# Performance work log

Measured on AMD Instinct MI355X. Metric: run time of the kernel, lower is better.

The kernel has to match this reference:

```python
import jax, jax.numpy as jnp
import numpy as np

VOCAB = 30522
EMB = 128
H = 128          # per-direction GRU hidden (text_hidden_size // 2)
TXT = 256        # text_hidden_size
VDIM = 1024      # visual_feature_dim
VHID = 256       # video_hidden_dim
ADIM = 256       # alignment_dim
REG = 0.05
N_ITERS = 10


def gru_seq(x, Wi, Wh, bi, bh):
    """PyTorch-convention GRU. x:(B,T,I), Wi:(3H,I), Wh:(3H,H). Returns (B,T,H)."""
    B, T, _ = x.shape
    Hd = Wh.shape[1]
    xg = jnp.einsum('bti,gi->btg', x, Wi) + bi  # precompute input gates (B,T,3H)

    def step(h, xg_t):
        hg = h @ Wh.T + bh
        xr, xz, xn = jnp.split(xg_t, 3, axis=-1)
        hr, hz, hn = jnp.split(hg, 3, axis=-1)
        r = jax.nn.sigmoid(xr + hr)
        z = jax.nn.sigmoid(xz + hz)
        n = jnp.tanh(xn + r * hn)
        h_new = (1.0 - z) * n + z * h
        return h_new, h_new

    h0 = jnp.zeros((B, Hd), x.dtype)
    _, hs = jax.lax.scan(step, h0, jnp.swapaxes(xg, 0, 1))
    return jnp.swapaxes(hs, 0, 1)


def mlp_scorer(x, W1, b1, w2, b2, act):
    h = act(jnp.einsum('bsd,hd->bsh', x, W1) + b1)
    return jax.nn.sigmoid(jnp.einsum('bsh,h->bs', h, w2) + b2)


def sinkhorn(E, V, reg=REG, num_iters=N_ITERS):
    B, K, _ = E.shape
    M = V.shape[1]
    En = E / (jnp.linalg.norm(E, axis=-1, keepdims=True) + 1e-12)
    Vn = V / (jnp.linalg.norm(V, axis=-1, keepdims=True) + 1e-12)
    C = 1.0 - jnp.einsum('bkd,bmd->bkm', En, Vn)
    Km = jnp.exp(-C / reg)
    mu = jnp.full((B, K), 1.0 / K, E.dtype)
    nu = jnp.full((B, M), 1.0 / M, E.dtype)
    u = jnp.full((B, K), 1.0 / K, E.dtype)
    v = jnp.full((B, M), 1.0 / M, E.dtype)
    for _ in range(num_iters):
        u = mu / (jnp.einsum('bkm,bm->bk', Km, v) + 1e-8)
        v = nu / (jnp.einsum('bkm,bk->bm', Km, u) + 1e-8)
    T = u[:, :, None] * Km * v[:, None, :]
    dist = jnp.sum(T * C) / B
    return dist, T


def setup_inputs() -> dict:
    key = jax.random.key(0)
    ks = jax.random.split(key, 24)
    B, S, W, M = 16, 128, 32, 256
    s = 0.02
    inp = {
        'input_ids': jax.random.randint(ks[0], (B, S, W), 0, VOCAB),
        'attention_mask': jnp.ones((B, S, W), jnp.int64 if jax.config.jax_enable_x64 else jnp.int32),
        'video_features': jax.random.normal(ks[1], (B, M, VDIM), jnp.float32),
        'emb': jax.random.normal(ks[2], (VOCAB, EMB), jnp.float32) * s,
        'gru_Wi_f': jax.random.normal(ks[3], (3 * H, EMB), jnp.float32) * s,
        'gru_Wh_f': jax.random.normal(ks[4], (3 * H, H), jnp.float32) * s,
        'gru_bi_f': jnp.zeros((3 * H,), jnp.float32),
        'gru_bh_f': jnp.zeros((3 * H,), jnp.float32),
        'gru_Wi_b': jax.random.normal(ks[5], (3 * H, EMB), jnp.float32) * s,
        'gru_Wh_b': jax.random.normal(ks[6], (3 * H, H), jnp.float32) * s,
        'gru_bi_b': jnp.zeros((3 * H,), jnp.float32),
        'gru_bh_b': jnp.zeros((3 * H,), jnp.float32),
        'tproj_W': jax.random.normal(ks[7], (ADIM, TXT), jnp.float32) * s,
        'tproj_b': jnp.zeros((ADIM,), jnp.float32),
        'vproj_W': jax.random.normal(ks[8], (ADIM, VDIM), jnp.float32) * s,
        'vproj_b': jnp.zeros((ADIM,), jnp.float32),
        'tsum_W1': jax.random.normal(ks[9], (H, TXT), jnp.float32) * s,
        'tsum_b1': jnp.zeros((H,), jnp.float32),
        'tsum_w2': jax.random.normal(ks[10], (H,), jnp.float32) * s,
        'tsum_b2': jnp.zeros((), jnp.float32),
        'vsum_W1': jax.random.normal(ks[11], (VHID, VDIM), jnp.float32) * s,
        'vsum_b1': jnp.zeros((VHID,), jnp.float32),
        'vsum_w2': jax.random.normal(ks[12], (VHID,), jnp.float32) * s,
        'vsum_b2': jnp.zeros((), jnp.float32),
        'vts_W1': jax.random.normal(ks[13], (VHID, VDIM), jnp.float32) * s,
        'vts_b1': jnp.zeros((VHID,), jnp.float32),
        'vts_w2': jax.random.normal(ks[14], (VHID,), jnp.float32) * s,
        'vts_b2': jnp.zeros((), jnp.float32),
    }
    return inp


def reference(input_ids, attention_mask, video_features, emb,
              gru_Wi_f, gru_Wh_f, gru_bi_f, gru_bh_f,
              gru_Wi_b, gru_Wh_b, gru_bi_b, gru_bh_b,
              tproj_W, tproj_b, vproj_W, vproj_b,
              tsum_W1, tsum_b1, tsum_w2, tsum_b2,
              vsum_W1, vsum_b1, vsum_w2, vsum_b2,
              vts_W1, vts_b1, vts_w2, vts_b2):
    B, S, W = input_ids.shape
    flat = input_ids.reshape(B * S, W)
    embeds = emb[flat]  # (B*S, W, EMB); padding_idx=0 row is just a table row here
    fwd = gru_seq(embeds, gru_Wi_f, gru_Wh_f, gru_bi_f, gru_bh_f)
    bwd = gru_seq(embeds[:, ::-1, :], gru_Wi_b, gru_Wh_b, gru_bi_b, gru_bh_b)[:, ::-1, :]
    gru_out = jnp.concatenate([fwd, bwd], axis=-1)  # (B*S, W, 2H)
    text_features = gru_out.mean(axis=1).reshape(B, S, TXT)

    text_seg_probs = jnp.zeros((B, S), text_features.dtype)
    video_seg_probs = mlp_scorer(video_features, vts_W1, vts_b1, vts_w2, vts_b2, jax.nn.relu)
    text_summ_probs = mlp_scorer(text_features, tsum_W1, tsum_b1, tsum_w2, tsum_b2, jnp.tanh)
    video_summ_probs = mlp_scorer(video_features, vsum_W1, vsum_b1, vsum_w2, vsum_b2, jnp.tanh)

    E_w = text_features * text_summ_probs[:, :, None]
    V_w = video_features * video_summ_probs[:, :, None]
    E_proj = jnp.einsum('bsd,ad->bsa', E_w, tproj_W) + tproj_b
    V_proj = jnp.einsum('bmd,ad->bma', V_w, vproj_W) + vproj_b

    ot_loss, T = sinkhorn(E_proj, V_proj)
    return (text_seg_probs, text_features, video_seg_probs, text_summ_probs,
            video_summ_probs, ot_loss, T)
```

## Files before the change

### kernel.cpp

```cpp
#include <hip/hip_runtime.h>
#include <hip/hip_bf16.h>

typedef unsigned short u16;
typedef __attribute__((ext_vector_type(8))) short short8;
typedef __attribute__((ext_vector_type(4))) float f32x4;

static __device__ __forceinline__ float bf2f(u16 x) {
    unsigned int u = ((unsigned int)x) << 16;
    return __uint_as_float(u);
}
static __device__ __forceinline__ u16 f2bf(float f) {
    unsigned int u = __float_as_uint(f);
    unsigned int r = (u + 0x7fffu + ((u >> 16) & 1u)) >> 16;
    return (u16)r;
}
static __device__ __forceinline__ float sigmoidf(float x) {
    return 1.0f / (1.0f + expf(-x));
}

__global__ void k_zero(float* __restrict__ out) {
    int t = blockIdx.x * 256 + threadIdx.x;
    if (t < 2048) out[t] = 0.0f;
    if (t == 0) out[536576] = 0.0f;
}

__global__ void k_cvte(const float* __restrict__ emb, const float* __restrict__ WiF,
                       const float* __restrict__ WiB, u16* __restrict__ dst) {
    long i4 = ((long)blockIdx.x * 256 + threadIdx.x) * 4;
    if (i4 >= 4005120) return;
    float4 v;
    if (i4 < 3906816) v = *(const float4*)(emb + i4);
    else if (i4 < 3955968) v = *(const float4*)(WiF + (i4 - 3906816));
    else v = *(const float4*)(WiB + (i4 - 3955968));
    ushort4 o;
    o.x = f2bf(v.x); o.y = f2bf(v.y); o.z = f2bf(v.z); o.w = f2bf(v.w);
    *(ushort4*)(dst + i4) = o;
}

__global__ __launch_bounds__(256) void k_xg2(const int* __restrict__ ids, const u16* __restrict__ embb,
                                             const u16* __restrict__ Wib, const float* __restrict__ bi,
                                             u16* __restrict__ xg) {
    __shared__ u16 As[128][40];
    __shared__ u16 Bs[128][40];
    const int t = threadIdx.x;
    const int m0 = blockIdx.x * 128, n0 = blockIdx.y * 128;
    const int w = t >> 6, l = t & 63;
    const int wr = w >> 1, wc = w & 1;
    const int lrow = l & 15, lk = (l >> 4) * 8;
    f32x4 acc[4][4] = {};
#pragma unroll
    for (int kk = 0; kk < 4; kk++) {
        const int k0 = kk * 32;
        int4 ra[2], rb[2];
#pragma unroll
        for (int it = 0; it < 2; it++) {
            int e = it * 256 + t;
            int row = e >> 2, c8 = (e & 3) * 8;
            int id = ids[m0 + row];
            ra[it] = *(const int4*)(embb + (long)id * 128 + k0 + c8);
            rb[it] = *(const int4*)(Wib + (long)(n0 + row) * 128 + k0 + c8);
        }
        __syncthreads();
#pragma unroll
        for (int it = 0; it < 2; it++) {
            int e = it * 256 + t;
            int row = e >> 2, c8 = (e & 3) * 8;
            *(int4*)&As[row][c8] = ra[it];
            *(int4*)&Bs[row][c8] = rb[it];
        }
        __syncthreads();
        short8 af[4], bf[4];
#pragma unroll
        for (int f = 0; f < 4; f++) {
            af[f] = *(const short8*)&As[wr * 64 + f * 16 + lrow][lk];
            bf[f] = *(const short8*)&Bs[wc * 64 + f * 16 + lrow][lk];
        }
#pragma unroll
        for (int fm = 0; fm < 4; fm++)
#pragma unroll
            for (int fn = 0; fn < 4; fn++)
                acc[fm][fn] = __builtin_amdgcn_mfma_f32_16x16x32_bf16(af[fm], bf[fn], acc[fm][fn], 0, 0, 0);
    }
    const int orow = (l >> 4) * 4, ocol = l & 15;
#pragma unroll
    for (int fm = 0; fm < 4; fm++)
#pragma unroll
        for (int fn = 0; fn < 4; fn++) {
            const int col = n0 + wc * 64 + fn * 16 + ocol;
            const float bbv = bi[col];
            const int row0 = m0 + wr * 64 + fm * 16 + orow;
#pragma unroll
            for (int r = 0; r < 4; r++)
                xg[(long)(row0 + r) * 384 + col] = f2bf(acc[fm][fn][r] + bbv);
        }
}

__global__ __launch_bounds__(256) void k_scan2(const u16* __restrict__ xg,
                                               const float* __restrict__ Wh,
                                               const float* __restrict__ bh,
                                               float* __restrict__ tf_out, int dir) {
    __shared__ u16 hbuf[2][16][136];
    const int t = threadIdx.x;
    const int w = t >> 6, l = t & 63;
    const int lr = l & 15, hi = l >> 4;
    const int seq0 = blockIdx.x * 8;

    short8 breg[3][2][4];
    float bb[3][2];
#pragma unroll
    for (int g = 0; g < 3; g++)
#pragma unroll
        for (int h2 = 0; h2 < 2; h2++) {
            const int ncol = g * 128 + w * 32 + h2 * 16 + lr;
            const float* wrow = Wh + (long)ncol * 128;
            bb[g][h2] = bh[ncol];
#pragma unroll
            for (int q = 0; q < 4; q++) {
                float4 a = *(const float4*)(wrow + q * 32 + hi * 8);
                float4 b = *(const float4*)(wrow + q * 32 + hi * 8 + 4);
                short8 s;
                s[0] = f2bf(a.x); s[1] = f2bf(a.y); s[2] = f2bf(a.z); s[3] = f2bf(a.w);
                s[4] = f2bf(b.x); s[5] = f2bf(b.y); s[6] = f2bf(b.z); s[7] = f2bf(b.w);
                breg[g][h2][q] = s;
            }
        }

    for (int i = t; i < 2176; i += 256) ((int*)hbuf)[i] = 0;

    float hreg[2][4] = {};
    float macc[2][4] = {};
    __syncthreads();

    for (int tt = 0; tt < 32; tt++) {
        const int tp = dir ? (31 - tt) : tt;
        const int cur = tt & 1;

        float xv[3][2][4];
        if (hi < 2) {
#pragma unroll
            for (int g = 0; g < 3; g++)
#pragma unroll
                for (int h2 = 0; h2 < 2; h2++)
#pragma unroll
                    for (int r = 0; r < 4; r++) {
                        const int m = hi * 4 + r;
                        xv[g][h2][r] = bf2f(xg[((long)(seq0 + m) * 32 + tp) * 384
                                               + g * 128 + w * 32 + h2 * 16 + lr]);
                    }
        }

        short8 af[4];
#pragma unroll
        for (int q = 0; q < 4; q++)
            af[q] = *(const short8*)&hbuf[cur][lr][q * 32 + hi * 8];

        f32x4 acc[3][2];
#pragma unroll
        for (int g = 0; g < 3; g++)
#pragma unroll
            for (int h2 = 0; h2 < 2; h2++) {
                f32x4 a = {0.f, 0.f, 0.f, 0.f};
#pragma unroll
                for (int q = 0; q < 4; q++)
                    a = __builtin_amdgcn_mfma_f32_16x16x32_bf16(af[q], breg[g][h2][q], a, 0, 0, 0);
                acc[g][h2] = a;
            }

        if (hi < 2) {
#pragma unroll
            for (int h2 = 0; h2 < 2; h2++)
#pragma unroll
                for (int r = 0; r < 4; r++) {
                    float rg = sigmoidf(xv[0][h2][r] + acc[0][h2][r] + bb[0][h2]);
                    float zg = sigmoidf(xv[1][h2][r] + acc[1][h2][r] + bb[1][h2]);
                    float ng = tanhf(xv[2][h2][r] + rg * (acc[2][h2][r] + bb[2][h2]));
                    float h = (1.0f - zg) * ng + zg * hreg[h2][r];
                    hreg[h2][r] = h;
                    macc[h2][r] += h;
                    hbuf[cur ^ 1][hi * 4 + r][w * 32 + h2 * 16 + lr] = f2bf(h);
                }
        }
        __syncthreads();
    }

    if (hi < 2) {
#pragma unroll
        for (int h2 = 0; h2 < 2; h2++)
#pragma unroll
            for (int r = 0; r < 4; r++)
                tf_out[(long)(seq0 + hi * 4 + r) * 256 + dir * 128 + w * 32 + h2 * 16 + lr]
                    = macc[h2][r] * (1.0f / 32.0f);
    }
}

__global__ void k_tsum(const float* __restrict__ tf, const float* __restrict__ W1,
                       const float* __restrict__ b1, const float* __restrict__ w2,
                       const float* __restrict__ b2, float* __restrict__ out) {
    __shared__ float x[256];
    __shared__ float wsum[2];
    const int row = blockIdx.x, t = threadIdx.x;
    x[t] = tf[(long)row * 256 + t];
    x[t + 128] = tf[(long)row * 256 + 128 + t];
    __syncthreads();
    float acc = 0.f;
    const float* w = W1 + (long)t * 256;
#pragma unroll 8
    for (int i = 0; i < 256; i += 4) {
        float4 w4 = *(const float4*)(w + i);
        acc += w4.x * x[i] + w4.y * x[i + 1] + w4.z * x[i + 2] + w4.w * x[i + 3];
    }
    float h = tanhf(acc + b1[t]) * w2[t];
    for (int o = 32; o > 0; o >>= 1) h += __shfl_xor(h, o);
    if ((t & 63) == 0) wsum[t >> 6] = h;
    __syncthreads();
    if (t == 0) out[row] = sigmoidf(wsum[0] + wsum[1] + b2[0]);
}

__global__ void k_cvt(const float* __restrict__ vf, const float* __restrict__ wa,
                      const float* __restrict__ wb2, const float* __restrict__ wc2,
                      u16* __restrict__ Xb, u16* __restrict__ Wb) {
    long gid = (long)blockIdx.x * 256 + threadIdx.x;
    long i4 = gid * 4;
    float4 v;
    u16* dst;
    if (i4 < 4194304) {
        v = *(const float4*)(vf + i4);
        dst = Xb + i4;
    } else {
        long j = i4 - 4194304;
        dst = Wb + j;
        if (j < 262144) v = *(const float4*)(wa + j);
        else if (j < 524288) v = *(const float4*)(wb2 + (j - 262144));
        else v = *(const float4*)(wc2 + (j - 524288));
    }
    ushort4 o;
    o.x = f2bf(v.x); o.y = f2bf(v.y); o.z = f2bf(v.z); o.w = f2bf(v.w);
    *(ushort4*)dst = o;
}

__global__ __launch_bounds__(256) void k_gemmv(const u16* __restrict__ Xb, const u16* __restrict__ Wb,
                                               float* __restrict__ G) {
    __shared__ u16 As[128][40];
    __shared__ u16 Bs[128][40];
    const int t = threadIdx.x;
    const int m0 = blockIdx.x * 128, n0 = blockIdx.y * 128;
    const int w = t >> 6, l = t & 63;
    const int wr = w >> 1, wc = w & 1;
    const int lrow = l & 15, lk = (l >> 4) * 8;
    f32x4 acc[4][4] = {};
    for (int kk = 0; kk < 32; kk++) {
        const int k0 = kk * 32;
        int4 ra[2], rb[2];
#pragma unroll
        for (int it = 0; it < 2; it++) {
            int e = it * 256 + t;
            int row = e >> 2, c8 = (e & 3) * 8;
            ra[it] = *(const int4*)(Xb + (long)(m0 + row) * 1024 + k0 + c8);
            rb[it] = *(const int4*)(Wb + (long)(n0 + row) * 1024 + k0 + c8);
        }
        __syncthreads();
#pragma unroll
        for (int it = 0; it < 2; it++) {
            int e = it * 256 + t;
            int row = e >> 2, c8 = (e & 3) * 8;
            *(int4*)&As[row][c8] = ra[it];
            *(int4*)&Bs[row][c8] = rb[it];
        }
        __syncthreads();
        short8 af[4], bf[4];
#pragma unroll
        for (int f = 0; f < 4; f++) {
            af[f] = *(const short8*)&As[wr * 64 + f * 16 + lrow][lk];
            bf[f] = *(const short8*)&Bs[wc * 64 + f * 16 + lrow][lk];
        }
#pragma unroll
        for (int fm = 0; fm < 4; fm++)
#pragma unroll
            for (int fn = 0; fn < 4; fn++)
                acc[fm][fn] = __builtin_amdgcn_mfma_f32_16x16x32_bf16(af[fm], bf[fn], acc[fm][fn], 0, 0, 0);
    }
    const int orow = (l >> 4) * 4, ocol = l & 15;
#pragma unroll
    for (int fm = 0; fm < 4; fm++)
#pragma unroll
        for (int fn = 0; fn < 4; fn++) {
            long base = (long)(m0 + wr * 64 + fm * 16 + orow) * 768 + n0 + wc * 64 + fn * 16 + ocol;
#pragma unroll
            for (int r = 0; r < 4; r++)
                G[base + (long)r * 768] = acc[fm][fn][r];
        }
}

__global__ void k_vepi(const float* __restrict__ G,
                       const float* __restrict__ bv, const float* __restrict__ w2v, const float* __restrict__ b2v,
                       const float* __restrict__ bt, const float* __restrict__ w2t, const float* __restrict__ b2t,
                       const float* __restrict__ vpb,
                       float* __restrict__ V, float* __restrict__ vsp, float* __restrict__ vseg) {
    const int r = blockIdx.x * 4 + (threadIdx.x >> 6);
    const int lane = threadIdx.x & 63;
    const float* g = G + (long)r * 768;
    float s1 = 0.f, s2 = 0.f;
#pragma unroll
    for (int c = 0; c < 4; c++) {
        int h = lane + c * 64;
        s1 += tanhf(g[h] + bv[h]) * w2v[h];
        s2 += fmaxf(g[256 + h] + bt[h], 0.0f) * w2t[h];
    }
    for (int o = 32; o > 0; o >>= 1) { s1 += __shfl_xor(s1, o); s2 += __shfl_xor(s2, o); }
    float p = sigmoidf(s1 + b2v[0]);
    if (lane == 0) {
        vsp[r] = p;
        vseg[r] = sigmoidf(s2 + b2t[0]);
    }
#pragma unroll
    for (int c = 0; c < 4; c++) {
        int a = lane + c * 64;
        V[(long)r * 256 + a] = vpb[a] + p * g[512 + a];
    }
}

__global__ void k_eproj(const float* __restrict__ tf, const float* __restrict__ tsp,
                        const float* __restrict__ W, const float* __restrict__ b,
                        float* __restrict__ E) {
    __shared__ float x[8][256];
    __shared__ float p[8];
    const int r0 = blockIdx.x * 8, t = threadIdx.x;
    const float4* src = (const float4*)(tf + (long)r0 * 256);
    for (int i = t; i < 512; i += 256) ((float4*)&x[0][0])[i] = src[i];
    if (t < 8) p[t] = tsp[r0 + t];
    __syncthreads();
    float acc[8] = {};
    const float* w = W + (long)t * 256;
    for (int i = 0; i < 256; i += 4) {
        float4 w4 = *(const float4*)(w + i);
#pragma unroll
        for (int r = 0; r < 8; r++) {
            float4 x4 = *(const float4*)&x[r][i];
            acc[r] += w4.x * x4.x + w4.y * x4.y + w4.z * x4.z + w4.w * x4.w;
        }
    }
    const float bb = b[t];
#pragma unroll
    for (int r = 0; r < 8; r++) E[(long)(r0 + r) * 256 + t] = bb + p[r] * acc[r];
}

__global__ void k_norm(float* __restrict__ E, float* __restrict__ V) {
    const int w = threadIdx.x >> 6, lane = threadIdx.x & 63;
    const int row = blockIdx.x * 4 + w;
    float* ptr = (row < 2048) ? (E + (long)row * 256) : (V + (long)(row - 2048) * 256);
    float4 v = ((float4*)ptr)[lane];
    float s = v.x * v.x + v.y * v.y + v.z * v.z + v.w * v.w;
    for (int o = 32; o > 0; o >>= 1) s += __shfl_xor(s, o);
    float sc = 1.0f / (sqrtf(s) + 1e-12f);
    v.x *= sc; v.y *= sc; v.z *= sc; v.w *= sc;
    ((float4*)ptr)[lane] = v;
}

__global__ void k_cost(const float* __restrict__ E, const float* __restrict__ V,
                       float* __restrict__ C, float* __restrict__ Km) {
    __shared__ float en[16][256];
    const int b = blockIdx.x, k0 = blockIdx.y * 16, t = threadIdx.x;
    const float4* esrc = (const float4*)(E + ((long)b * 128 + k0) * 256);
    for (int i = t; i < 1024; i += 256) ((float4*)&en[0][0])[i] = esrc[i];
    __syncthreads();
    float acc[16] = {};
    const float* vrow = V + ((long)b * 256 + t) * 256;
    for (int i = 0; i < 256; i += 4) {
        float4 v4 = *(const float4*)(vrow + i);
#pragma unroll
        for (int k = 0; k < 16; k++) {
            float4 e4 = *(const float4*)&en[k][i];
            acc[k] += e4.x * v4.x + e4.y * v4.y + e4.z * v4.z + e4.w * v4.w;
        }
    }
#pragma unroll
    for (int k = 0; k < 16; k++) {
        float c = 1.0f - acc[k];
        long idx = (long)b * 32768 + (long)(k0 + k) * 256 + t;
        C[idx] = c;
        Km[idx] = expf(-20.0f * c);
    }
}

__global__ void k_sink(const float* __restrict__ C, const float* __restrict__ Km,
                       float* __restrict__ T, float* __restrict__ loss) {
    __shared__ float u[128];
    __shared__ float v[256];
    __shared__ float red[8];
    const int b = blockIdx.x, t = threadIdx.x;
    const float* Kb = Km + (long)b * 32768;
    const float* Cb = C + (long)b * 32768;
    if (t < 128) u[t] = 1.0f / 128.0f;
    if (t < 256) v[t] = 1.0f / 256.0f;
    __syncthreads();
    for (int it = 0; it < 10; it++) {
        {
            const int k = t >> 2, q = t & 3;
            const float* kr = Kb + (long)k * 256 + q * 64;
            float s = 0.f;
#pragma unroll 4
            for (int m = 0; m < 64; m += 4) {
                float4 k4 = *(const float4*)(kr + m);
                float4 vv = *(const float4*)&v[q * 64 + m];
                s += k4.x * vv.x + k4.y * vv.y + k4.z * vv.z + k4.w * vv.w;
            }
            s += __shfl_xor(s, 1);
            s += __shfl_xor(s, 2);
            float un = (1.0f / 128.0f) / (s + 1e-8f);
            u[k] = un;
            __syncthreads();
        }
        {
            const int m = t >> 1, q = t & 1;
            float s = 0.f;
            for (int k = 0; k < 64; k += 4) {
                float4 u4 = *(const float4*)&u[q * 64 + k];
                s += Kb[(long)(q * 64 + k + 0) * 256 + m] * u4.x;
                s += Kb[(long)(q * 64 + k + 1) * 256 + m] * u4.y;
                s += Kb[(long)(q * 64 + k + 2) * 256 + m] * u4.z;
                s += Kb[(long)(q * 64 + k + 3) * 256 + m] * u4.w;
            }
            s += __shfl_xor(s, 1);
            float vn = (1.0f / 256.0f) / (s + 1e-8f);
            v[m] = vn;
            __syncthreads();
        }
    }
    float part = 0.f;
    for (int i = 0; i < 64; i++) {
        int idx = i * 512 + t;
        int k = idx >> 8, m = idx & 255;
        float tv = u[k] * Kb[idx] * v[m];
        T[(long)b * 32768 + idx] = tv;
        part += tv * Cb[idx];
    }
    for (int o = 32; o > 0; o >>= 1) part += __shfl_xor(part, o);
    if ((t & 63) == 0) red[t >> 6] = part;
    __syncthreads();
    if (t == 0) {
        float s = red[0] + red[1] + red[2] + red[3] + red[4] + red[5] + red[6] + red[7];
        atomicAdd(loss, s * (1.0f / 16.0f));
    }
}

extern "C" void kernel_launch(void* const* d_in, const int* in_sizes, int n_in,
                              void* d_out, int out_size, void* d_ws, size_t ws_size,
                              hipStream_t stream) {
    const int*   ids  = (const int*)d_in[0];
    const float* vf   = (const float*)d_in[2];
    const float* emb  = (const float*)d_in[3];
    const float* WiF  = (const float*)d_in[4];
    const float* WhF  = (const float*)d_in[5];
    const float* biF  = (const float*)d_in[6];
    const float* bhF  = (const float*)d_in[7];
    const float* WiB  = (const float*)d_in[8];
    const float* WhB  = (const float*)d_in[9];
    const float* biB  = (const float*)d_in[10];
    const float* bhB  = (const float*)d_in[11];
    const float* tpW  = (const float*)d_in[12];
    const float* tpb  = (const float*)d_in[13];
    const float* vpW  = (const float*)d_in[14];
    const float* vpb  = (const float*)d_in[15];
    const float* tsW1 = (const float*)d_in[16];
    const float* tsb1 = (const float*)d_in[17];
    const float* tsw2 = (const float*)d_in[18];
    const float* tsb2 = (const float*)d_in[19];
    const float* vsW1 = (const float*)d_in[20];
    const float* vsb1 = (const float*)d_in[21];
    const float* vsw2 = (const float*)d_in[22];
    const float* vsb2 = (const float*)d_in[23];
    const float* vtW1 = (const float*)d_in[24];
    const float* vtb1 = (const float*)d_in[25];
    const float* vtw2 = (const float*)d_in[26];
    const float* vtb2 = (const float*)d_in[27];
    float* out = (float*)d_out;

    char* ws = (char*)d_ws;
    u16*   XG = (u16*)ws;
    u16*   Xb = (u16*)ws;
    u16*   Wb = (u16*)(ws + 8388608);
    float* G  = (float*)(ws + 9961472);
    u16*   embb = (u16*)(ws + 50331648);
    u16*   WibF = embb + 3906816;
    u16*   WibB = embb + 3955968;
    float* E  = (float*)(ws + 50331648);
    float* V  = (float*)(ws + 52428800);
    float* C  = (float*)(ws + 56623104);
    float* Km = (float*)(ws + 58720256);

    float* tf   = out + 2048;
    float* vseg = out + 526336;
    float* tsp  = out + 530432;
    float* vsp  = out + 532480;
    float* loss = out + 536576;
    float* T    = out + 536577;

    k_zero<<<8, 256, 0, stream>>>(out);

    k_cvte<<<3912, 256, 0, stream>>>(emb, WiF, WiB, embb);
    k_xg2<<<dim3(512, 3), 256, 0, stream>>>(ids, embb, WibF, biF, XG);
    k_scan2<<<256, 256, 0, stream>>>(XG, WhF, bhF, tf, 0);
    k_xg2<<<dim3(512, 3), 256, 0, stream>>>(ids, embb, WibB, biB, XG);
    k_scan2<<<256, 256, 0, stream>>>(XG, WhB, bhB, tf, 1);

    k_cvt<<<4864, 256, 0, stream>>>(vf, vsW1, vtW1, vpW, Xb, Wb);
    k_gemmv<<<dim3(32, 6), 256, 0, stream>>>(Xb, Wb, G);
    k_vepi<<<1024, 256, 0, stream>>>(G, vsb1, vsw2, vsb2, vtb1, vtw2, vtb2, vpb, V, vsp, vseg);

    k_tsum<<<2048, 128, 0, stream>>>(tf, tsW1, tsb1, tsw2, tsb2, tsp);
    k_eproj<<<256, 256, 0, stream>>>(tf, tsp, tpW, tpb, E);
    k_norm<<<1536, 256, 0, stream>>>(E, V);
    k_cost<<<dim3(16, 8), 256, 0, stream>>>(E, V, C, Km);
    k_sink<<<16, 512, 0, stream>>>(C, Km, T, loss);
}
```

Before: 572.7 us.

## Restructure GRU scan with time-major xg, LDS prefetch, 8 waves, fast math

The input-gate projection is now written time-major, so each scan step reads one contiguous slab of 8 sequences. The scan block is doubled to 512 threads (8 waves), each owning 16 hidden columns. The next timestep's gates are prefetched into a double-buffered LDS tile while the current step computes, which takes scattered global loads off the serial recurrence. Sigmoid, tanh and exp switch to fast-intrinsic versions throughout, trading some accuracy for shorter latency.

```diff
diff --git a/kernel.cpp b/kernel.cpp
--- a/kernel.cpp
+++ b/kernel.cpp
@@ -16,6 +16,12 @@
 }
 static __device__ __forceinline__ float sigmoidf(float x) {
     return 1.0f / (1.0f + expf(-x));
+}
+static __device__ __forceinline__ float fsig(float x) {
+    return __fdividef(1.0f, 1.0f + __expf(-x));
+}
+static __device__ __forceinline__ float ftanh(float x) {
+    return 1.0f - __fdividef(2.0f, 1.0f + __expf(2.0f * x));
 }
 
 __global__ void k_zero(float* __restrict__ out) {
@@ -39,7 +45,7 @@
 
 __global__ __launch_bounds__(256) void k_xg2(const int* __restrict__ ids, const u16* __restrict__ embb,
                                              const u16* __restrict__ Wib, const float* __restrict__ bi,
-                                             u16* __restrict__ xg) {
+                                             u16* __restrict__ xgt) {
     __shared__ u16 As[128][40];
     __shared__ u16 Bs[128][40];
     const int t = threadIdx.x;
@@ -90,106 +96,100 @@
             const float bbv = bi[col];
             const int row0 = m0 + wr * 64 + fm * 16 + orow;
 #pragma unroll
-            for (int r = 0; r < 4; r++)
-                xg[(long)(row0 + r) * 384 + col] = f2bf(acc[fm][fn][r] + bbv);
-        }
-}
-
-__global__ __launch_bounds__(256) void k_scan2(const u16* __restrict__ xg,
+            for (int r = 0; r < 4; r++) {
+                const int mrow = row0 + r;
+                xgt[((long)(mrow & 31) * 2048 + (mrow >> 5)) * 384 + col]
+                    = f2bf(acc[fm][fn][r] + bbv);
+            }
+        }
+}
+
+__global__ __launch_bounds__(512) void k_scan3(const u16* __restrict__ xgt,
                                                const float* __restrict__ Wh,
                                                const float* __restrict__ bh,
                                                float* __restrict__ tf_out, int dir) {
-    __shared__ u16 hbuf[2][16][136];
+    __shared__ u16 hbuf[2][16][140];
+    __shared__ u16 xbuf[2][8][392];
     const int t = threadIdx.x;
     const int w = t >> 6, l = t & 63;
     const int lr = l & 15, hi = l >> 4;
     const int seq0 = blockIdx.x * 8;
 
-    short8 breg[3][2][4];
-    float bb[3][2];
-#pragma unroll
-    for (int g = 0; g < 3; g++)
-#pragma unroll
-        for (int h2 = 0; h2 < 2; h2++) {
-            const int ncol = g * 128 + w * 32 + h2 * 16 + lr;
-            const float* wrow = Wh + (long)ncol * 128;
-            bb[g][h2] = bh[ncol];
-#pragma unroll
-            for (int q = 0; q < 4; q++) {
-                float4 a = *(const float4*)(wrow + q * 32 + hi * 8);
-                float4 b = *(const float4*)(wrow + q * 32 + hi * 8 + 4);
-                short8 s;
-                s[0] = f2bf(a.x); s[1] = f2bf(a.y); s[2] = f2bf(a.z); s[3] = f2bf(a.w);
-                s[4] = f2bf(b.x); s[5] = f2bf(b.y); s[6] = f2bf(b.z); s[7] = f2bf(b.w);
-                breg[g][h2][q] = s;
-            }
-        }
-
-    for (int i = t; i < 2176; i += 256) ((int*)hbuf)[i] = 0;
-
-    float hreg[2][4] = {};
-    float macc[2][4] = {};
+    short8 breg[3][4];
+    float bb[3];
+#pragma unroll
+    for (int g = 0; g < 3; g++) {
+        const int ncol = g * 128 + w * 16 + lr;
+        const float* wrow = Wh + (long)ncol * 128;
+        bb[g] = bh[ncol];
+#pragma unroll
+        for (int q = 0; q < 4; q++) {
+            float4 a = *(const float4*)(wrow + q * 32 + hi * 8);
+            float4 b = *(const float4*)(wrow + q * 32 + hi * 8 + 4);
+            short8 s;
+            s[0] = f2bf(a.x); s[1] = f2bf(a.y); s[2] = f2bf(a.z); s[3] = f2bf(a.w);
+            s[4] = f2bf(b.x); s[5] = f2bf(b.y); s[6] = f2bf(b.z); s[7] = f2bf(b.w);
+            breg[g][q] = s;
+        }
+    }
+    for (int i = t; i < 2240; i += 512) ((int*)hbuf)[i] = 0;
+    const int seqr = t / 48, part = t % 48;
+    if (t < 384) {
+        const int tp0 = dir ? 31 : 0;
+        *(int4*)&xbuf[0][seqr][part * 8] =
+            *(const int4*)(xgt + ((long)tp0 * 2048 + seq0 + seqr) * 384 + part * 8);
+    }
+    float hreg[4] = {0.f, 0.f, 0.f, 0.f};
+    float macc[4] = {0.f, 0.f, 0.f, 0.f};
     __syncthreads();
 
     for (int tt = 0; tt < 32; tt++) {
-        const int tp = dir ? (31 - tt) : tt;
         const int cur = tt & 1;
-
-        float xv[3][2][4];
-        if (hi < 2) {
-#pragma unroll
-            for (int g = 0; g < 3; g++)
-#pragma unroll
-                for (int h2 = 0; h2 < 2; h2++)
-#pragma unroll
-                    for (int r = 0; r < 4; r++) {
-                        const int m = hi * 4 + r;
-                        xv[g][h2][r] = bf2f(xg[((long)(seq0 + m) * 32 + tp) * 384
-                                               + g * 128 + w * 32 + h2 * 16 + lr]);
-                    }
-        }
-
+        int4 pre;
+        const bool do_pre = (tt < 31) && (t < 384);
+        if (do_pre) {
+            const int tpn = dir ? (30 - tt) : (tt + 1);
+            pre = *(const int4*)(xgt + ((long)tpn * 2048 + seq0 + seqr) * 384 + part * 8);
+        }
         short8 af[4];
 #pragma unroll
         for (int q = 0; q < 4; q++)
             af[q] = *(const short8*)&hbuf[cur][lr][q * 32 + hi * 8];
-
-        f32x4 acc[3][2];
-#pragma unroll
-        for (int g = 0; g < 3; g++)
-#pragma unroll
-            for (int h2 = 0; h2 < 2; h2++) {
-                f32x4 a = {0.f, 0.f, 0.f, 0.f};
-#pragma unroll
-                for (int q = 0; q < 4; q++)
-                    a = __builtin_amdgcn_mfma_f32_16x16x32_bf16(af[q], breg[g][h2][q], a, 0, 0, 0);
-                acc[g][h2] = a;
+        f32x4 acc[3];
+#pragma unroll
+        for (int g = 0; g < 3; g++) {
+            f32x4 a = {0.f, 0.f, 0.f, 0.f};
+#pragma unroll
+            for (int q = 0; q < 4; q++)
+                a = __builtin_amdgcn_mfma_f32_16x16x32_bf16(af[q], breg[g][q], a, 0, 0, 0);
+            acc[g] = a;
+        }
+        if (hi < 2) {
+            const int c = w * 16 + lr;
+#pragma unroll
+            for (int r = 0; r < 4; r++) {
+                const int m = hi * 4 + r;
+                float xr = bf2f(xbuf[cur][m][c]);
+                float xz = bf2f(xbuf[cur][m][128 + c]);
+                float xn = bf2f(xbuf[cur][m][256 + c]);
+                float rg = fsig(xr + acc[0][r] + bb[0]);
+                float zg = fsig(xz + acc[1][r] + bb[1]);
+                float ng = ftanh(xn + rg * (acc[2][r] + bb[2]));
+                float h = (1.0f - zg) * ng + zg * hreg[r];
+                hreg[r] = h;
+                macc[r] += h;
+                hbuf[cur ^ 1][m][c] = f2bf(h);
             }
-
-        if (hi < 2) {
-#pragma unroll
-            for (int h2 = 0; h2 < 2; h2++)
-#pragma unroll
-                for (int r = 0; r < 4; r++) {
-                    float rg = sigmoidf(xv[0][h2][r] + acc[0][h2][r] + bb[0][h2]);
-                    float zg = sigmoidf(xv[1][h2][r] + acc[1][h2][r] + bb[1][h2]);
-                    float ng = tanhf(xv[2][h2][r] + rg * (acc[2][h2][r] + bb[2][h2]));
-                    float h = (1.0f - zg) * ng + zg * hreg[h2][r];
-                    hreg[h2][r] = h;
-                    macc[h2][r] += h;
-                    hbuf[cur ^ 1][hi * 4 + r][w * 32 + h2 * 16 + lr] = f2bf(h);
-                }
-        }
+        }
+        if (do_pre) *(int4*)&xbuf[cur ^ 1][seqr][part * 8] = pre;
         __syncthreads();
     }
 
     if (hi < 2) {
 #pragma unroll
-        for (int h2 = 0; h2 < 2; h2++)
-#pragma unroll
-            for (int r = 0; r < 4; r++)
-                tf_out[(long)(seq0 + hi * 4 + r) * 256 + dir * 128 + w * 32 + h2 * 16 + lr]
-                    = macc[h2][r] * (1.0f / 32.0f);
+        for (int r = 0; r < 4; r++)
+            tf_out[(long)(seq0 + hi * 4 + r) * 256 + dir * 128 + w * 16 + lr]
+                = macc[r] * (1.0f / 32.0f);
     }
 }
 
@@ -209,11 +209,11 @@
         float4 w4 = *(const float4*)(w + i);
         acc += w4.x * x[i] + w4.y * x[i + 1] + w4.z * x[i + 2] + w4.w * x[i + 3];
     }
-    float h = tanhf(acc + b1[t]) * w2[t];
+    float h = ftanh(acc + b1[t]) * w2[t];
     for (int o = 32; o > 0; o >>= 1) h += __shfl_xor(h, o);
     if ((t & 63) == 0) wsum[t >> 6] = h;
     __syncthreads();
-    if (t == 0) out[row] = sigmoidf(wsum[0] + wsum[1] + b2[0]);
+    if (t == 0) out[row] = fsig(wsum[0] + wsum[1] + b2[0]);
 }
 
 __global__ void k_cvt(const float* __restrict__ vf, const float* __restrict__ wa,
@@ -303,14 +303,14 @@
 #pragma unroll
     for (int c = 0; c < 4; c++) {
         int h = lane + c * 64;
-        s1 += tanhf(g[h] + bv[h]) * w2v[h];
+        s1 += ftanh(g[h] + bv[h]) * w2v[h];
         s2 += fmaxf(g[256 + h] + bt[h], 0.0f) * w2t[h];
     }
     for (int o = 32; o > 0; o >>= 1) { s1 += __shfl_xor(s1, o); s2 += __shfl_xor(s2, o); }
-    float p = sigmoidf(s1 + b2v[0]);
+    float p = fsig(s1 + b2v[0]);
     if (lane == 0) {
         vsp[r] = p;
-        vseg[r] = sigmoidf(s2 + b2t[0]);
+        vseg[r] = fsig(s2 + b2t[0]);
     }
 #pragma unroll
     for (int c = 0; c < 4; c++) {
@@ -378,7 +378,7 @@
         float c = 1.0f - acc[k];
         long idx = (long)b * 32768 + (long)(k0 + k) * 256 + t;
         C[idx] = c;
-        Km[idx] = expf(-20.0f * c);
+        Km[idx] = __expf(-20.0f * c);
     }
 }
 
@@ -476,7 +476,7 @@
     float* out = (float*)d_out;
 
     char* ws = (char*)d_ws;
-    u16*   XG = (u16*)ws;
+    u16*   XGT = (u16*)ws;
     u16*   Xb = (u16*)ws;
     u16*   Wb = (u16*)(ws + 8388608);
     float* G  = (float*)(ws + 9961472);
@@ -498,10 +498,10 @@
     k_zero<<<8, 256, 0, stream>>>(out);
 
     k_cvte<<<3912, 256, 0, stream>>>(emb, WiF, WiB, embb);
-    k_xg2<<<dim3(512, 3), 256, 0, stream>>>(ids, embb, WibF, biF, XG);
-    k_scan2<<<256, 256, 0, stream>>>(XG, WhF, bhF, tf, 0);
-    k_xg2<<<dim3(512, 3), 256, 0, stream>>>(ids, embb, WibB, biB, XG);
-    k_scan2<<<256, 256, 0, stream>>>(XG, WhB, bhB, tf, 1);
+    k_xg2<<<dim3(512, 3), 256, 0, stream>>>(ids, embb, WibF, biF, XGT);
+    k_scan3<<<256, 512, 0, stream>>>(XGT, WhF, bhF, tf, 0);
+    k_xg2<<<dim3(512, 3), 256, 0, stream>>>(ids, embb, WibB, biB, XGT);
+    k_scan3<<<256, 512, 0, stream>>>(XGT, WhB, bhB, tf, 1);
 
     k_cvt<<<4864, 256, 0, stream>>>(vf, vsW1, vtW1, vpW, Xb, Wb);
     k_gemmv<<<dim3(32, 6), 256, 0, stream>>>(Xb, Wb, G);
```

New measurement: 510.2 us. 10.9% less time.
